# Kernel tuning notes

Hardware: AMD Instinct MI355X
Metric: run time of the kernel (lower is better)

The kernel has to match this reference:

```python
import jax, jax.numpy as jnp
import numpy as np

N_SRC1, N_DST1, N_DST2 = 200000, 50000, 10000
E1, E2 = 2000000, 400000
IN_F, H_F, N_CLS = 128, 256, 47


def setup_inputs() -> dict:
    key = jax.random.key(0)
    ks = jax.random.split(key, 10)
    x = jax.random.normal(ks[0], (N_SRC1, IN_F), dtype=jnp.float32)
    W_self1 = jax.random.normal(ks[1], (IN_F, H_F), dtype=jnp.float32) * (1.0 / np.sqrt(IN_F))
    W_neigh1 = jax.random.normal(ks[2], (IN_F, H_F), dtype=jnp.float32) * (1.0 / np.sqrt(IN_F))
    b1 = jnp.zeros((H_F,), dtype=jnp.float32)
    W_self2 = jax.random.normal(ks[3], (H_F, N_CLS), dtype=jnp.float32) * (1.0 / np.sqrt(H_F))
    W_neigh2 = jax.random.normal(ks[4], (H_F, N_CLS), dtype=jnp.float32) * (1.0 / np.sqrt(H_F))
    b2 = jnp.zeros((N_CLS,), dtype=jnp.float32)
    src1 = jax.random.randint(ks[5], (E1,), 0, N_SRC1, dtype=jnp.int64)
    dst1 = jnp.sort(jax.random.randint(ks[6], (E1,), 0, N_DST1, dtype=jnp.int64))
    src2 = jax.random.randint(ks[7], (E2,), 0, N_DST1, dtype=jnp.int64)
    dst2 = jnp.sort(jax.random.randint(ks[8], (E2,), 0, N_DST2, dtype=jnp.int64))
    return {"x": x, "W_self1": W_self1, "W_neigh1": W_neigh1, "b1": b1,
            "W_self2": W_self2, "W_neigh2": W_neigh2, "b2": b2,
            "src1": src1, "dst1": dst1, "src2": src2, "dst2": dst2,
            "n_dst1": N_DST1, "n_dst2": N_DST2}


def _sage_mean(h_src, h_dst, src, dst, n_dst, W_self, W_neigh, b):
    # mean neighbor aggregation: gather src feats, segment-sum onto dst, divide by in-degree
    msum = jax.ops.segment_sum(h_src[src], dst, num_segments=n_dst)  # [n_dst, F]
    deg = jax.ops.segment_sum(jnp.ones(src.shape, h_src.dtype), dst, num_segments=n_dst)
    h_neigh = msum / jnp.maximum(deg, 1.0)[:, None]
    return h_dst @ W_self + h_neigh @ W_neigh + b


def reference(x, W_self1, W_neigh1, b1, W_self2, W_neigh2, b2,
              src1, dst1, src2, dst2, n_dst1, n_dst2):
    # layer 1 (dst nodes are the prefix of src nodes, DGL MFG convention)
    h = _sage_mean(x, x[:n_dst1], src1, dst1, n_dst1, W_self1, W_neigh1, b1)
    h = jax.nn.relu(h)  # dropout = identity (eval mode)
    # layer 2
    out = _sage_mean(h, h[:n_dst2], src2, dst2, n_dst2, W_self2, W_neigh2, b2)
    return out
```

## Files before the change

kernel.cpp:

```cpp
#include <hip/hip_runtime.h>

constexpr int N_DST1 = 50000;
constexpr int N_DST2 = 10000;
constexpr int E1     = 2000000;
constexpr int E2     = 400000;
constexpr int IN_F   = 128;
constexpr int H_F    = 256;
constexpr int N_CLS  = 47;

constexpr size_t RP1_OFF = 0;
constexpr size_t RP2_OFF = 204800;
constexpr size_t BPS_OFF = 245760;
constexpr size_t BPN_OFF = 311296;
constexpr size_t BP2_OFF = 376832;
constexpr size_t X8_OFF  = 430080;
constexpr size_t HN1_OFF = 26030080;
constexpr size_t HB_OFF  = 38830080;
constexpr size_t H8_OFF  = 64430080;
constexpr size_t HN2_OFF = 77230080;

using f32x4  = __attribute__((ext_vector_type(4))) float;
using f32x2  = __attribute__((ext_vector_type(2))) float;
using short8 = __attribute__((ext_vector_type(8))) short;

__device__ __forceinline__ ushort f2bf(float f) {
    union { float f; unsigned u; } v; v.f = f;
    unsigned u = v.u;
    return (ushort)((u + 0x7fffu + ((u >> 16) & 1u)) >> 16);
}

constexpr int CAST_BLKS = 200000 * IN_F / 8 / 256;
constexpr int PACK_BLKS = 44;
constexpr int RP_BLKS   = (N_DST1 + N_DST2 + 2 + 255) / 256;

__global__ __launch_bounds__(256) void setup_all(
    const float* __restrict__ x, unsigned char* __restrict__ x8,
    const float* __restrict__ Ws1, const float* __restrict__ Wn1,
    const float* __restrict__ Ws2, const float* __restrict__ Wn2,
    ushort* __restrict__ bps, ushort* __restrict__ bpn, ushort* __restrict__ bp2,
    const int* __restrict__ dst1, const int* __restrict__ dst2,
    int* __restrict__ rp1, int* __restrict__ rp2) {
    int b = blockIdx.x;
    if (b < CAST_BLKS) {
        int i = b * 256 + threadIdx.x;
        float4 v0 = ((const float4*)x)[2 * i];
        float4 v1 = ((const float4*)x)[2 * i + 1];
        int p0 = __builtin_amdgcn_cvt_pk_fp8_f32(v0.x, v0.y, 0, false);
        p0     = __builtin_amdgcn_cvt_pk_fp8_f32(v0.z, v0.w, p0, true);
        int p1 = __builtin_amdgcn_cvt_pk_fp8_f32(v1.x, v1.y, 0, false);
        p1     = __builtin_amdgcn_cvt_pk_fp8_f32(v1.z, v1.w, p1, true);
        uint2 o; o.x = (unsigned)p0; o.y = (unsigned)p1;
        ((uint2*)x8)[i] = o;
    } else if (b < CAST_BLKS + PACK_BLKS) {
        int pb = b - CAST_BLKS;
        if (pb < 32) {
            const float* W = (pb < 16) ? Ws1 : Wn1;
            ushort* P      = (pb < 16) ? bps : bpn;
            int idx = (pb & 15) * 256 + threadIdx.x;
            int lane = idx & 63, kb = (idx >> 6) & 3, nb = idx >> 8;
            int n  = nb * 16 + (lane & 15);
            int k0 = kb * 32 + ((lane >> 4) * 8);
            ushort tmp[8];
#pragma unroll
            for (int j = 0; j < 8; ++j) tmp[j] = f2bf(W[(k0 + j) * H_F + n]);
            ((uint4*)P)[idx] = *(uint4*)tmp;
        } else {
            int idx = (pb - 32) * 256 + threadIdx.x;
            if (idx < 3072) {
                int lane = idx & 63, rem = idx >> 6;
                int nb = rem % 3, kb = rem / 3;
                int col = nb * 16 + (lane & 15);
                int k0  = (kb & 7) * 32 + ((lane >> 4) * 8);
                const float* W = (kb < 8) ? Ws2 : Wn2;
                ushort tmp[8];
#pragma unroll
                for (int j = 0; j < 8; ++j)
                    tmp[j] = (col < N_CLS) ? f2bf(W[(k0 + j) * N_CLS + col]) : (ushort)0;
                ((uint4*)bp2)[(kb * 3 + nb) * 64 + lane] = *(uint4*)tmp;
            }
        }
    } else {
        int idx = (b - CAST_BLKS - PACK_BLKS) * 256 + threadIdx.x;
        const int* dst; int* rp; int E; int target;
        if (idx <= N_DST1) { dst = dst1; rp = rp1; E = E1; target = idx; }
        else if (idx <= N_DST1 + 1 + N_DST2) {
            dst = dst2; rp = rp2; E = E2; target = idx - (N_DST1 + 1);
        } else return;
        int lo = 0, hi = E;
        while (lo < hi) {
            int mid = (lo + hi) >> 1;
            if (dst[mid] < target) lo = mid + 1; else hi = mid;
        }
        rp[target] = lo;
    }
}

__global__ __launch_bounds__(64) void agg1b(const unsigned char* __restrict__ x8,
                                            const int* __restrict__ src,
                                            const int* __restrict__ rp,
                                            ushort* __restrict__ hn) {
    int d = blockIdx.x, t = threadIdx.x;
    int s = rp[d], e = rp[d + 1];
    const unsigned* x1 = (const unsigned*)x8;
    int half = t >> 5, li = t & 31;
    float a0 = 0.f, a1 = 0.f, a2 = 0.f, a3 = 0.f;
    int deg = e - s;
    int npairs = deg >> 1;
    int j = 0;
    for (; j + 4 <= npairs; j += 4) {
        int b0 = s + 2 * j;
        int i0 = src[b0],     i1 = src[b0 + 1], i2 = src[b0 + 2], i3 = src[b0 + 3];
        int i4 = src[b0 + 4], i5 = src[b0 + 5], i6 = src[b0 + 6], i7 = src[b0 + 7];
        unsigned v0 = x1[(half ? i1 : i0) * 32 + li];
        unsigned v1 = x1[(half ? i3 : i2) * 32 + li];
        unsigned v2 = x1[(half ? i5 : i4) * 32 + li];
        unsigned v3 = x1[(half ? i7 : i6) * 32 + li];
#pragma unroll
        for (int q = 0; q < 4; ++q) {
            unsigned v = (q == 0) ? v0 : (q == 1) ? v1 : (q == 2) ? v2 : v3;
            f32x2 f0 = __builtin_amdgcn_cvt_pk_f32_fp8((int)v, false);
            f32x2 f1 = __builtin_amdgcn_cvt_pk_f32_fp8((int)v, true);
            a0 += f0[0]; a1 += f0[1]; a2 += f1[0]; a3 += f1[1];
        }
    }
    for (; j < npairs; ++j) {
        int b0 = s + 2 * j;
        int i0 = src[b0], i1 = src[b0 + 1];
        unsigned v = x1[(half ? i1 : i0) * 32 + li];
        f32x2 f0 = __builtin_amdgcn_cvt_pk_f32_fp8((int)v, false);
        f32x2 f1 = __builtin_amdgcn_cvt_pk_f32_fp8((int)v, true);
        a0 += f0[0]; a1 += f0[1]; a2 += f1[0]; a3 += f1[1];
    }
    if (deg & 1) {
        int it = src[e - 1];
        if (half == 0) {
            unsigned v = x1[it * 32 + li];
            f32x2 f0 = __builtin_amdgcn_cvt_pk_f32_fp8((int)v, false);
            f32x2 f1 = __builtin_amdgcn_cvt_pk_f32_fp8((int)v, true);
            a0 += f0[0]; a1 += f0[1]; a2 += f1[0]; a3 += f1[1];
        }
    }
    float c0 = a0 + __shfl(a0, li + 32);
    float c1 = a1 + __shfl(a1, li + 32);
    float c2 = a2 + __shfl(a2, li + 32);
    float c3 = a3 + __shfl(a3, li + 32);
    if (t < 32) {
        float inv = 1.f / fmaxf((float)deg, 1.f);
        uint2 o;
        o.x = (unsigned)f2bf(c0 * inv) | ((unsigned)f2bf(c1 * inv) << 16);
        o.y = (unsigned)f2bf(c2 * inv) | ((unsigned)f2bf(c3 * inv) << 16);
        ((uint2*)hn)[d * 32 + li] = o;
    }
}

__global__ __launch_bounds__(64) void agg2b(const unsigned char* __restrict__ h8,
                                            const int* __restrict__ src,
                                            const int* __restrict__ rp,
                                            ushort* __restrict__ hn) {
    int d = blockIdx.x, t = threadIdx.x;
    int s = rp[d], e = rp[d + 1];
    const uint2* h2 = (const uint2*)h8;
    int half = t >> 5, li = t & 31;
    float a[8] = {};
    int deg = e - s;
    int npairs = deg >> 1;
    int j = 0;
    for (; j + 2 <= npairs; j += 2) {
        int b0 = s + 2 * j;
        int i0 = src[b0], i1 = src[b0 + 1], i2 = src[b0 + 2], i3 = src[b0 + 3];
        uint2 v0 = h2[(half ? i1 : i0) * 32 + li];
        uint2 v1 = h2[(half ? i3 : i2) * 32 + li];
#pragma unroll
        for (int q = 0; q < 2; ++q) {
            uint2 v = q ? v1 : v0;
            f32x2 f0 = __builtin_amdgcn_cvt_pk_f32_fp8((int)v.x, false);
            f32x2 f1 = __builtin_amdgcn_cvt_pk_f32_fp8((int)v.x, true);
            f32x2 f2 = __builtin_amdgcn_cvt_pk_f32_fp8((int)v.y, false);
            f32x2 f3 = __builtin_amdgcn_cvt_pk_f32_fp8((int)v.y, true);
            a[0] += f0[0]; a[1] += f0[1]; a[2] += f1[0]; a[3] += f1[1];
            a[4] += f2[0]; a[5] += f2[1]; a[6] += f3[0]; a[7] += f3[1];
        }
    }
    for (; j < npairs; ++j) {
        int b0 = s + 2 * j;
        int i0 = src[b0], i1 = src[b0 + 1];
        uint2 v = h2[(half ? i1 : i0) * 32 + li];
        f32x2 f0 = __builtin_amdgcn_cvt_pk_f32_fp8((int)v.x, false);
        f32x2 f1 = __builtin_amdgcn_cvt_pk_f32_fp8((int)v.x, true);
        f32x2 f2 = __builtin_amdgcn_cvt_pk_f32_fp8((int)v.y, false);
        f32x2 f3 = __builtin_amdgcn_cvt_pk_f32_fp8((int)v.y, true);
        a[0] += f0[0]; a[1] += f0[1]; a[2] += f1[0]; a[3] += f1[1];
        a[4] += f2[0]; a[5] += f2[1]; a[6] += f3[0]; a[7] += f3[1];
    }
    if (deg & 1) {
        int it = src[e - 1];
        if (half == 0) {
            uint2 v = h2[it * 32 + li];
            f32x2 f0 = __builtin_amdgcn_cvt_pk_f32_fp8((int)v.x, false);
            f32x2 f1 = __builtin_amdgcn_cvt_pk_f32_fp8((int)v.x, true);
            f32x2 f2 = __builtin_amdgcn_cvt_pk_f32_fp8((int)v.y, false);
            f32x2 f3 = __builtin_amdgcn_cvt_pk_f32_fp8((int)v.y, true);
            a[0] += f0[0]; a[1] += f0[1]; a[2] += f1[0]; a[3] += f1[1];
            a[4] += f2[0]; a[5] += f2[1]; a[6] += f3[0]; a[7] += f3[1];
        }
    }
    float c[8];
#pragma unroll
    for (int q = 0; q < 8; ++q) c[q] = a[q] + __shfl(a[q], li + 32);
    if (t < 32) {
        float inv = 1.f / fmaxf((float)deg, 1.f);
        uint4 o;
        o.x = (unsigned)f2bf(c[0] * inv) | ((unsigned)f2bf(c[1] * inv) << 16);
        o.y = (unsigned)f2bf(c[2] * inv) | ((unsigned)f2bf(c[3] * inv) << 16);
        o.z = (unsigned)f2bf(c[4] * inv) | ((unsigned)f2bf(c[5] * inv) << 16);
        o.w = (unsigned)f2bf(c[6] * inv) | ((unsigned)f2bf(c[7] * inv) << 16);
        ((uint4*)hn)[d * 32 + li] = o;
    }
}

__global__ __launch_bounds__(256) void gemm1_mfma(
    const float* __restrict__ x, const ushort* __restrict__ hn1,
    const ushort* __restrict__ BpS, const ushort* __restrict__ BpN,
    const float* __restrict__ b1, ushort* __restrict__ hb,
    unsigned char* __restrict__ h8) {
    __shared__ ushort bsm[16 * 64 * 8];
    int tid = threadIdx.x;
    int wave = tid >> 6, lane = tid & 63;
    int m0 = (blockIdx.x * 4 + wave) * 16;
    int mrow = m0 + (lane & 15);
    bool active = (m0 < N_DST1);
    if (mrow >= N_DST1) mrow = 0;
    int koff = (lane >> 4) * 8;

    f32x4 acc[16];
#pragma unroll
    for (int nb = 0; nb < 16; ++nb) acc[nb] = (f32x4){0.f, 0.f, 0.f, 0.f};

    for (int ph = 0; ph < 2; ++ph) {
        const uint4* Pg = (const uint4*)((ph == 0) ? BpS : BpN);
        const float*  Af = x   + (size_t)mrow * IN_F;
        const ushort* Ah = hn1 + (size_t)mrow * IN_F;
        for (int kb = 0; kb < 4; ++kb) {
            __syncthreads();
#pragma unroll
            for (int i = 0; i < 4; ++i) {
                int u = tid + 256 * i;
                int nb = u >> 6, l6 = u & 63;
                ((uint4*)bsm)[u] = Pg[(nb * 4 + kb) * 64 + l6];
            }
            __syncthreads();
            short8 a;
            if (ph == 0) {
                float4 a0 = *(const float4*)(Af + kb * 32 + koff);
                float4 a1 = *(const float4*)(Af + kb * 32 + koff + 4);
                a[0] = (short)f2bf(a0.x); a[1] = (short)f2bf(a0.y);
                a[2] = (short)f2bf(a0.z); a[3] = (short)f2bf(a0.w);
                a[4] = (short)f2bf(a1.x); a[5] = (short)f2bf(a1.y);
                a[6] = (short)f2bf(a1.z); a[7] = (short)f2bf(a1.w);
            } else {
                a = *(const short8*)(Ah + kb * 32 + koff);
            }
#pragma unroll
            for (int nb = 0; nb < 16; ++nb) {
                short8 b = *(const short8*)&bsm[(nb * 64 + lane) * 8];
                acc[nb] = __builtin_amdgcn_mfma_f32_16x16x32_bf16(a, b, acc[nb], 0, 0, 0);
            }
        }
    }
    if (!active) return;
    int crow0 = m0 + (lane >> 4) * 4;
    int ccol  = lane & 15;
#pragma unroll
    for (int nb = 0; nb < 16; ++nb) {
        float bias = b1[nb * 16 + ccol];
#pragma unroll
        for (int r = 0; r < 4; ++r) {
            int row = crow0 + r;
            if (row < N_DST1) {
                float v = fmaxf(acc[nb][r] + bias, 0.f);
                size_t col = (size_t)nb * 16 + ccol;
                hb[(size_t)row * H_F + col] = f2bf(v);
                int p = __builtin_amdgcn_cvt_pk_fp8_f32(v, v, 0, false);
                h8[(size_t)row * H_F + col] = (unsigned char)(p & 0xff);
            }
        }
    }
}

__global__ __launch_bounds__(256) void gemm2_mfma(
    const ushort* __restrict__ hb, const ushort* __restrict__ hn2,
    const ushort* __restrict__ P2, const float* __restrict__ b2,
    float* __restrict__ out) {
    int tid = threadIdx.x;
    int wave = tid >> 6, lane = tid & 63;
    int m0 = (blockIdx.x * 4 + wave) * 16;
    if (m0 >= N_DST2) return;
    int mrow = m0 + (lane & 15);
    int koff = (lane >> 4) * 8;

    f32x4 acc[3];
#pragma unroll
    for (int nb = 0; nb < 3; ++nb) acc[nb] = (f32x4){0.f, 0.f, 0.f, 0.f};

#pragma unroll
    for (int kb = 0; kb < 16; ++kb) {
        const ushort* A = (kb < 8)
            ? (hb  + (size_t)mrow * H_F + kb * 32 + koff)
            : (hn2 + (size_t)mrow * H_F + (kb - 8) * 32 + koff);
        short8 a = *(const short8*)A;
#pragma unroll
        for (int nb = 0; nb < 3; ++nb) {
            short8 b = *(const short8*)(P2 + ((size_t)(kb * 3 + nb) * 64 + lane) * 8);
            acc[nb] = __builtin_amdgcn_mfma_f32_16x16x32_bf16(a, b, acc[nb], 0, 0, 0);
        }
    }
    int crow0 = m0 + (lane >> 4) * 4;
    int ccol  = lane & 15;
#pragma unroll
    for (int nb = 0; nb < 3; ++nb) {
        int col = nb * 16 + ccol;
        if (col < N_CLS) {
            float bias = b2[col];
#pragma unroll
            for (int r = 0; r < 4; ++r)
                out[(size_t)(crow0 + r) * N_CLS + col] = acc[nb][r] + bias;
        }
    }
}

extern "C" void kernel_launch(void* const* d_in, const int* in_sizes, int n_in,
                              void* d_out, int out_size, void* d_ws, size_t ws_size,
                              hipStream_t stream) {
    const float* x   = (const float*)d_in[0];
    const float* Ws1 = (const float*)d_in[1];
    const float* Wn1 = (const float*)d_in[2];
    const float* b1  = (const float*)d_in[3];
    const float* Ws2 = (const float*)d_in[4];
    const float* Wn2 = (const float*)d_in[5];
    const float* b2  = (const float*)d_in[6];
    const int* src1  = (const int*)d_in[7];
    const int* dst1  = (const int*)d_in[8];
    const int* src2  = (const int*)d_in[9];
    const int* dst2  = (const int*)d_in[10];
    float* out = (float*)d_out;

    char* ws = (char*)d_ws;
    int*           rp1 = (int*)(ws + RP1_OFF);
    int*           rp2 = (int*)(ws + RP2_OFF);
    ushort*        bps = (ushort*)(ws + BPS_OFF);
    ushort*        bpn = (ushort*)(ws + BPN_OFF);
    ushort*        bp2 = (ushort*)(ws + BP2_OFF);
    unsigned char* x8  = (unsigned char*)(ws + X8_OFF);
    ushort*        hn1 = (ushort*)(ws + HN1_OFF);
    ushort*        hb  = (ushort*)(ws + HB_OFF);
    unsigned char* h8  = (unsigned char*)(ws + H8_OFF);
    ushort*        hn2 = (ushort*)(ws + HN2_OFF);

    setup_all<<<CAST_BLKS + PACK_BLKS + RP_BLKS, 256, 0, stream>>>(
        x, x8, Ws1, Wn1, Ws2, Wn2, bps, bpn, bp2, dst1, dst2, rp1, rp2);
    agg1b<<<N_DST1, 64, 0, stream>>>(x8, src1, rp1, hn1);
    gemm1_mfma<<<(N_DST1 / 16 + 3) / 4, 256, 0, stream>>>(x, hn1, bps, bpn, b1, hb, h8);
    agg2b<<<N_DST2, 64, 0, stream>>>(h8, src2, rp2, hn2);
    gemm2_mfma<<<(N_DST2 / 16 + 3) / 4, 256, 0, stream>>>(hb, hn2, bp2, b2, out);
}
```

Measured before the change: 306.6 us.

## Fuse neighbor aggregation into per-layer MFMA GEMM kernels via LDS tiles

Merges the layer-1 aggregation and GEMM into one kernel, and does the same for layer 2. Each wave now aggregates its 16 destination rows one after another into an LDS A-tile, then runs the MFMA GEMM from that tile. This removes the hn1/hn2 global round trips and two kernel launches. The self-feature bf16 copy hb is now written only for the rows layer 2 needs. In exchange, the latency-bound gather runs with far fewer waves in flight (782 blocks of 256 threads instead of 50000 single-wave blocks), and each wave handles its rows serially, so load-latency hiding may suffer.

```diff
diff --git a/kernel.cpp b/kernel.cpp
--- a/kernel.cpp
+++ b/kernel.cpp
@@ -14,10 +14,8 @@
 constexpr size_t BPN_OFF = 311296;
 constexpr size_t BP2_OFF = 376832;
 constexpr size_t X8_OFF  = 430080;
-constexpr size_t HN1_OFF = 26030080;
-constexpr size_t HB_OFF  = 38830080;
-constexpr size_t H8_OFF  = 64430080;
-constexpr size_t HN2_OFF = 77230080;
+constexpr size_t HB_OFF  = 26030080;
+constexpr size_t H8_OFF  = 31150080;
 
 using f32x4  = __attribute__((ext_vector_type(4))) float;
 using f32x2  = __attribute__((ext_vector_type(2))) float;
@@ -95,84 +93,167 @@
     }
 }
 
-__global__ __launch_bounds__(64) void agg1b(const unsigned char* __restrict__ x8,
-                                            const int* __restrict__ src,
-                                            const int* __restrict__ rp,
-                                            ushort* __restrict__ hn) {
-    int d = blockIdx.x, t = threadIdx.x;
-    int s = rp[d], e = rp[d + 1];
+__global__ __launch_bounds__(256) void layer1(
+    const float* __restrict__ x, const unsigned char* __restrict__ x8,
+    const int* __restrict__ src, const int* __restrict__ rp,
+    const ushort* __restrict__ BpS, const ushort* __restrict__ BpN,
+    const float* __restrict__ b1,
+    ushort* __restrict__ hb, unsigned char* __restrict__ h8) {
+    __shared__ ushort At[4][16 * 136];
+    __shared__ ushort bsm[16 * 64 * 8];
+    int tid = threadIdx.x, wave = tid >> 6, lane = tid & 63;
+    int m0 = blockIdx.x * 64 + wave * 16;
+    bool active = (m0 < N_DST1);
+    int half = lane >> 5, li = lane & 31;
+    ushort* Atile = At[wave];
     const unsigned* x1 = (const unsigned*)x8;
-    int half = t >> 5, li = t & 31;
-    float a0 = 0.f, a1 = 0.f, a2 = 0.f, a3 = 0.f;
-    int deg = e - s;
-    int npairs = deg >> 1;
-    int j = 0;
-    for (; j + 4 <= npairs; j += 4) {
-        int b0 = s + 2 * j;
-        int i0 = src[b0],     i1 = src[b0 + 1], i2 = src[b0 + 2], i3 = src[b0 + 3];
-        int i4 = src[b0 + 4], i5 = src[b0 + 5], i6 = src[b0 + 6], i7 = src[b0 + 7];
-        unsigned v0 = x1[(half ? i1 : i0) * 32 + li];
-        unsigned v1 = x1[(half ? i3 : i2) * 32 + li];
-        unsigned v2 = x1[(half ? i5 : i4) * 32 + li];
-        unsigned v3 = x1[(half ? i7 : i6) * 32 + li];
-#pragma unroll
-        for (int q = 0; q < 4; ++q) {
-            unsigned v = (q == 0) ? v0 : (q == 1) ? v1 : (q == 2) ? v2 : v3;
-            f32x2 f0 = __builtin_amdgcn_cvt_pk_f32_fp8((int)v, false);
-            f32x2 f1 = __builtin_amdgcn_cvt_pk_f32_fp8((int)v, true);
-            a0 += f0[0]; a1 += f0[1]; a2 += f1[0]; a3 += f1[1];
-        }
-    }
-    for (; j < npairs; ++j) {
-        int b0 = s + 2 * j;
-        int i0 = src[b0], i1 = src[b0 + 1];
-        unsigned v = x1[(half ? i1 : i0) * 32 + li];
-        f32x2 f0 = __builtin_amdgcn_cvt_pk_f32_fp8((int)v, false);
-        f32x2 f1 = __builtin_amdgcn_cvt_pk_f32_fp8((int)v, true);
-        a0 += f0[0]; a1 += f0[1]; a2 += f1[0]; a3 += f1[1];
-    }
-    if (deg & 1) {
-        int it = src[e - 1];
-        if (half == 0) {
-            unsigned v = x1[it * 32 + li];
-            f32x2 f0 = __builtin_amdgcn_cvt_pk_f32_fp8((int)v, false);
-            f32x2 f1 = __builtin_amdgcn_cvt_pk_f32_fp8((int)v, true);
-            a0 += f0[0]; a1 += f0[1]; a2 += f1[0]; a3 += f1[1];
-        }
-    }
-    float c0 = a0 + __shfl(a0, li + 32);
-    float c1 = a1 + __shfl(a1, li + 32);
-    float c2 = a2 + __shfl(a2, li + 32);
-    float c3 = a3 + __shfl(a3, li + 32);
-    if (t < 32) {
-        float inv = 1.f / fmaxf((float)deg, 1.f);
-        uint2 o;
-        o.x = (unsigned)f2bf(c0 * inv) | ((unsigned)f2bf(c1 * inv) << 16);
-        o.y = (unsigned)f2bf(c2 * inv) | ((unsigned)f2bf(c3 * inv) << 16);
-        ((uint2*)hn)[d * 32 + li] = o;
-    }
-}
-
-__global__ __launch_bounds__(64) void agg2b(const unsigned char* __restrict__ h8,
-                                            const int* __restrict__ src,
-                                            const int* __restrict__ rp,
-                                            ushort* __restrict__ hn) {
-    int d = blockIdx.x, t = threadIdx.x;
-    int s = rp[d], e = rp[d + 1];
+
+    if (active) {
+        for (int m = 0; m < 16; ++m) {
+            int d = m0 + m;
+            int s = rp[d], e = rp[d + 1];
+            int deg = e - s;
+            float a0 = 0.f, a1 = 0.f, a2 = 0.f, a3 = 0.f;
+            int npairs = deg >> 1;
+            int j = 0;
+            for (; j + 4 <= npairs; j += 4) {
+                int b0 = s + 2 * j;
+                int i0 = src[b0],     i1 = src[b0 + 1], i2 = src[b0 + 2], i3 = src[b0 + 3];
+                int i4 = src[b0 + 4], i5 = src[b0 + 5], i6 = src[b0 + 6], i7 = src[b0 + 7];
+                unsigned v0 = x1[(half ? i1 : i0) * 32 + li];
+                unsigned v1 = x1[(half ? i3 : i2) * 32 + li];
+                unsigned v2 = x1[(half ? i5 : i4) * 32 + li];
+                unsigned v3 = x1[(half ? i7 : i6) * 32 + li];
+#pragma unroll
+                for (int q = 0; q < 4; ++q) {
+                    unsigned v = (q == 0) ? v0 : (q == 1) ? v1 : (q == 2) ? v2 : v3;
+                    f32x2 f0 = __builtin_amdgcn_cvt_pk_f32_fp8((int)v, false);
+                    f32x2 f1 = __builtin_amdgcn_cvt_pk_f32_fp8((int)v, true);
+                    a0 += f0[0]; a1 += f0[1]; a2 += f1[0]; a3 += f1[1];
+                }
+            }
+            for (; j < npairs; ++j) {
+                int b0 = s + 2 * j;
+                int i0 = src[b0], i1 = src[b0 + 1];
+                unsigned v = x1[(half ? i1 : i0) * 32 + li];
+                f32x2 f0 = __builtin_amdgcn_cvt_pk_f32_fp8((int)v, false);
+                f32x2 f1 = __builtin_amdgcn_cvt_pk_f32_fp8((int)v, true);
+                a0 += f0[0]; a1 += f0[1]; a2 += f1[0]; a3 += f1[1];
+            }
+            if ((deg & 1) && half == 0) {
+                unsigned v = x1[src[e - 1] * 32 + li];
+                f32x2 f0 = __builtin_amdgcn_cvt_pk_f32_fp8((int)v, false);
+                f32x2 f1 = __builtin_amdgcn_cvt_pk_f32_fp8((int)v, true);
+                a0 += f0[0]; a1 += f0[1]; a2 += f1[0]; a3 += f1[1];
+            }
+            float c0 = a0 + __shfl(a0, li + 32);
+            float c1 = a1 + __shfl(a1, li + 32);
+            float c2 = a2 + __shfl(a2, li + 32);
+            float c3 = a3 + __shfl(a3, li + 32);
+            if (lane < 32) {
+                float inv = 1.f / fmaxf((float)deg, 1.f);
+                uint2 o;
+                o.x = (unsigned)f2bf(c0 * inv) | ((unsigned)f2bf(c1 * inv) << 16);
+                o.y = (unsigned)f2bf(c2 * inv) | ((unsigned)f2bf(c3 * inv) << 16);
+                *(uint2*)&Atile[m * 136 + li * 4] = o;
+            }
+        }
+    }
+
+    f32x4 acc[16];
+#pragma unroll
+    for (int nb = 0; nb < 16; ++nb) acc[nb] = (f32x4){0.f, 0.f, 0.f, 0.f};
+    int mloc = lane & 15;
+    int koff = (lane >> 4) * 8;
+    const float* Af = x + (size_t)(m0 + mloc) * IN_F;
+
+    for (int ph = 0; ph < 2; ++ph) {
+        const uint4* Pg = (const uint4*)((ph == 0) ? BpS : BpN);
+        for (int kb = 0; kb < 4; ++kb) {
+            __syncthreads();
+#pragma unroll
+            for (int i = 0; i < 4; ++i) {
+                int u = tid + 256 * i;
+                int nb = u >> 6, l6 = u & 63;
+                ((uint4*)bsm)[u] = Pg[(nb * 4 + kb) * 64 + l6];
+            }
+            __syncthreads();
+            short8 a;
+            if (ph == 0) {
+                float4 q0 = *(const float4*)(Af + kb * 32 + koff);
+                float4 q1 = *(const float4*)(Af + kb * 32 + koff + 4);
+                a[0] = (short)f2bf(q0.x); a[1] = (short)f2bf(q0.y);
+                a[2] = (short)f2bf(q0.z); a[3] = (short)f2bf(q0.w);
+                a[4] = (short)f2bf(q1.x); a[5] = (short)f2bf(q1.y);
+                a[6] = (short)f2bf(q1.z); a[7] = (short)f2bf(q1.w);
+            } else {
+                a = *(const short8*)&Atile[mloc * 136 + kb * 32 + koff];
+            }
+#pragma unroll
+            for (int nb = 0; nb < 16; ++nb) {
+                short8 b = *(const short8*)&bsm[(nb * 64 + lane) * 8];
+                acc[nb] = __builtin_amdgcn_mfma_f32_16x16x32_bf16(a, b, acc[nb], 0, 0, 0);
+            }
+        }
+    }
+    if (!active) return;
+    int crow0 = m0 + (lane >> 4) * 4;
+    int ccol  = lane & 15;
+#pragma unroll
+    for (int nb = 0; nb < 16; ++nb) {
+        float bias = b1[nb * 16 + ccol];
+#pragma unroll
+        for (int r = 0; r < 4; ++r) {
+            float v = fmaxf(acc[nb][r] + bias, 0.f);
+            int row = crow0 + r;
+            size_t col = (size_t)nb * 16 + ccol;
+            int p = __builtin_amdgcn_cvt_pk_fp8_f32(v, v, 0, false);
+            h8[(size_t)row * H_F + col] = (unsigned char)(p & 0xff);
+            if (row < N_DST2) hb[(size_t)row * H_F + col] = f2bf(v);
+        }
+    }
+}
+
+__global__ __launch_bounds__(256) void layer2(
+    const ushort* __restrict__ hb, const unsigned char* __restrict__ h8,
+    const int* __restrict__ src, const int* __restrict__ rp,
+    const ushort* __restrict__ P2, const float* __restrict__ b2,
+    float* __restrict__ out) {
+    __shared__ ushort At[4][16 * 264];
+    int tid = threadIdx.x, wave = tid >> 6, lane = tid & 63;
+    int m0 = blockIdx.x * 64 + wave * 16;
+    if (m0 >= N_DST2) return;
+    int half = lane >> 5, li = lane & 31;
+    ushort* Atile = At[wave];
     const uint2* h2 = (const uint2*)h8;
-    int half = t >> 5, li = t & 31;
-    float a[8] = {};
-    int deg = e - s;
-    int npairs = deg >> 1;
-    int j = 0;
-    for (; j + 2 <= npairs; j += 2) {
-        int b0 = s + 2 * j;
-        int i0 = src[b0], i1 = src[b0 + 1], i2 = src[b0 + 2], i3 = src[b0 + 3];
-        uint2 v0 = h2[(half ? i1 : i0) * 32 + li];
-        uint2 v1 = h2[(half ? i3 : i2) * 32 + li];
-#pragma unroll
-        for (int q = 0; q < 2; ++q) {
-            uint2 v = q ? v1 : v0;
+
+    for (int m = 0; m < 16; ++m) {
+        int d = m0 + m;
+        int s = rp[d], e = rp[d + 1];
+        int deg = e - s;
+        float a[8] = {};
+        int npairs = deg >> 1;
+        int j = 0;
+        for (; j + 2 <= npairs; j += 2) {
+            int b0 = s + 2 * j;
+            int i0 = src[b0], i1 = src[b0 + 1], i2 = src[b0 + 2], i3 = src[b0 + 3];
+            uint2 v0 = h2[(half ? i1 : i0) * 32 + li];
+            uint2 v1 = h2[(half ? i3 : i2) * 32 + li];
+#pragma unroll
+            for (int q = 0; q < 2; ++q) {
+                uint2 v = q ? v1 : v0;
+                f32x2 f0 = __builtin_amdgcn_cvt_pk_f32_fp8((int)v.x, false);
+                f32x2 f1 = __builtin_amdgcn_cvt_pk_f32_fp8((int)v.x, true);
+                f32x2 f2 = __builtin_amdgcn_cvt_pk_f32_fp8((int)v.y, false);
+                f32x2 f3 = __builtin_amdgcn_cvt_pk_f32_fp8((int)v.y, true);
+                a[0] += f0[0]; a[1] += f0[1]; a[2] += f1[0]; a[3] += f1[1];
+                a[4] += f2[0]; a[5] += f2[1]; a[6] += f3[0]; a[7] += f3[1];
+            }
+        }
+        for (; j < npairs; ++j) {
+            int b0 = s + 2 * j;
+            int i0 = src[b0], i1 = src[b0 + 1];
+            uint2 v = h2[(half ? i1 : i0) * 32 + li];
             f32x2 f0 = __builtin_amdgcn_cvt_pk_f32_fp8((int)v.x, false);
             f32x2 f1 = __builtin_amdgcn_cvt_pk_f32_fp8((int)v.x, true);
             f32x2 f2 = __builtin_amdgcn_cvt_pk_f32_fp8((int)v.y, false);
@@ -180,22 +261,8 @@
             a[0] += f0[0]; a[1] += f0[1]; a[2] += f1[0]; a[3] += f1[1];
             a[4] += f2[0]; a[5] += f2[1]; a[6] += f3[0]; a[7] += f3[1];
         }
-    }
-    for (; j < npairs; ++j) {
-        int b0 = s + 2 * j;
-        int i0 = src[b0], i1 = src[b0 + 1];
-        uint2 v = h2[(half ? i1 : i0) * 32 + li];
-        f32x2 f0 = __builtin_amdgcn_cvt_pk_f32_fp8((int)v.x, false);
-        f32x2 f1 = __builtin_amdgcn_cvt_pk_f32_fp8((int)v.x, true);
-        f32x2 f2 = __builtin_amdgcn_cvt_pk_f32_fp8((int)v.y, false);
-        f32x2 f3 = __builtin_amdgcn_cvt_pk_f32_fp8((int)v.y, true);
-        a[0] += f0[0]; a[1] += f0[1]; a[2] += f1[0]; a[3] += f1[1];
-        a[4] += f2[0]; a[5] += f2[1]; a[6] += f3[0]; a[7] += f3[1];
-    }
-    if (deg & 1) {
-        int it = src[e - 1];
-        if (half == 0) {
-            uint2 v = h2[it * 32 + li];
+        if ((deg & 1) && half == 0) {
+            uint2 v = h2[src[e - 1] * 32 + li];
             f32x2 f0 = __builtin_amdgcn_cvt_pk_f32_fp8((int)v.x, false);
             f32x2 f1 = __builtin_amdgcn_cvt_pk_f32_fp8((int)v.x, true);
             f32x2 f2 = __builtin_amdgcn_cvt_pk_f32_fp8((int)v.y, false);
@@ -203,111 +270,31 @@
             a[0] += f0[0]; a[1] += f0[1]; a[2] += f1[0]; a[3] += f1[1];
             a[4] += f2[0]; a[5] += f2[1]; a[6] += f3[0]; a[7] += f3[1];
         }
-    }
-    float c[8];
-#pragma unroll
-    for (int q = 0; q < 8; ++q) c[q] = a[q] + __shfl(a[q], li + 32);
-    if (t < 32) {
-        float inv = 1.f / fmaxf((float)deg, 1.f);
-        uint4 o;
-        o.x = (unsigned)f2bf(c[0] * inv) | ((unsigned)f2bf(c[1] * inv) << 16);
-        o.y = (unsigned)f2bf(c[2] * inv) | ((unsigned)f2bf(c[3] * inv) << 16);
-        o.z = (unsigned)f2bf(c[4] * inv) | ((unsigned)f2bf(c[5] * inv) << 16);
-        o.w = (unsigned)f2bf(c[6] * inv) | ((unsigned)f2bf(c[7] * inv) << 16);
-        ((uint4*)hn)[d * 32 + li] = o;
-    }
-}
-
-__global__ __launch_bounds__(256) void gemm1_mfma(
-    const float* __restrict__ x, const ushort* __restrict__ hn1,
-    const ushort* __restrict__ BpS, const ushort* __restrict__ BpN,
-    const float* __restrict__ b1, ushort* __restrict__ hb,
-    unsigned char* __restrict__ h8) {
-    __shared__ ushort bsm[16 * 64 * 8];
-    int tid = threadIdx.x;
-    int wave = tid >> 6, lane = tid & 63;
-    int m0 = (blockIdx.x * 4 + wave) * 16;
-    int mrow = m0 + (lane & 15);
-    bool active = (m0 < N_DST1);
-    if (mrow >= N_DST1) mrow = 0;
+        float c[8];
+#pragma unroll
+        for (int q = 0; q < 8; ++q) c[q] = a[q] + __shfl(a[q], li + 32);
+        if (lane < 32) {
+            float inv = 1.f / fmaxf((float)deg, 1.f);
+            uint4 o;
+            o.x = (unsigned)f2bf(c[0] * inv) | ((unsigned)f2bf(c[1] * inv) << 16);
+            o.y = (unsigned)f2bf(c[2] * inv) | ((unsigned)f2bf(c[3] * inv) << 16);
+            o.z = (unsigned)f2bf(c[4] * inv) | ((unsigned)f2bf(c[5] * inv) << 16);
+            o.w = (unsigned)f2bf(c[6] * inv) | ((unsigned)f2bf(c[7] * inv) << 16);
+            *(uint4*)&Atile[m * 264 + li * 8] = o;
+        }
+    }
+
+    f32x4 acc[3];
+#pragma unroll
+    for (int nb = 0; nb < 3; ++nb) acc[nb] = (f32x4){0.f, 0.f, 0.f, 0.f};
+    int mloc = lane & 15;
     int koff = (lane >> 4) * 8;
-
-    f32x4 acc[16];
-#pragma unroll
-    for (int nb = 0; nb < 16; ++nb) acc[nb] = (f32x4){0.f, 0.f, 0.f, 0.f};
-
-    for (int ph = 0; ph < 2; ++ph) {
-        const uint4* Pg = (const uint4*)((ph == 0) ? BpS : BpN);
-        const float*  Af = x   + (size_t)mrow * IN_F;
-        const ushort* Ah = hn1 + (size_t)mrow * IN_F;
-        for (int kb = 0; kb < 4; ++kb) {
-            __syncthreads();
-#pragma unroll
-            for (int i = 0; i < 4; ++i) {
-                int u = tid + 256 * i;
-                int nb = u >> 6, l6 = u & 63;
-                ((uint4*)bsm)[u] = Pg[(nb * 4 + kb) * 64 + l6];
-            }
-            __syncthreads();
-            short8 a;
-            if (ph == 0) {
-                float4 a0 = *(const float4*)(Af + kb * 32 + koff);
-                float4 a1 = *(const float4*)(Af + kb * 32 + koff + 4);
-                a[0] = (short)f2bf(a0.x); a[1] = (short)f2bf(a0.y);
-                a[2] = (short)f2bf(a0.z); a[3] = (short)f2bf(a0.w);
-                a[4] = (short)f2bf(a1.x); a[5] = (short)f2bf(a1.y);
-                a[6] = (short)f2bf(a1.z); a[7] = (short)f2bf(a1.w);
-            } else {
-                a = *(const short8*)(Ah + kb * 32 + koff);
-            }
-#pragma unroll
-            for (int nb = 0; nb < 16; ++nb) {
-                short8 b = *(const short8*)&bsm[(nb * 64 + lane) * 8];
-                acc[nb] = __builtin_amdgcn_mfma_f32_16x16x32_bf16(a, b, acc[nb], 0, 0, 0);
-            }
-        }
-    }
-    if (!active) return;
-    int crow0 = m0 + (lane >> 4) * 4;
-    int ccol  = lane & 15;
-#pragma unroll
-    for (int nb = 0; nb < 16; ++nb) {
-        float bias = b1[nb * 16 + ccol];
-#pragma unroll
-        for (int r = 0; r < 4; ++r) {
-            int row = crow0 + r;
-            if (row < N_DST1) {
-                float v = fmaxf(acc[nb][r] + bias, 0.f);
-                size_t col = (size_t)nb * 16 + ccol;
-                hb[(size_t)row * H_F + col] = f2bf(v);
-                int p = __builtin_amdgcn_cvt_pk_fp8_f32(v, v, 0, false);
-                h8[(size_t)row * H_F + col] = (unsigned char)(p & 0xff);
-            }
-        }
-    }
-}
-
-__global__ __launch_bounds__(256) void gemm2_mfma(
-    const ushort* __restrict__ hb, const ushort* __restrict__ hn2,
-    const ushort* __restrict__ P2, const float* __restrict__ b2,
-    float* __restrict__ out) {
-    int tid = threadIdx.x;
-    int wave = tid >> 6, lane = tid & 63;
-    int m0 = (blockIdx.x * 4 + wave) * 16;
-    if (m0 >= N_DST2) return;
-    int mrow = m0 + (lane & 15);
-    int koff = (lane >> 4) * 8;
-
-    f32x4 acc[3];
-#pragma unroll
-    for (int nb = 0; nb < 3; ++nb) acc[nb] = (f32x4){0.f, 0.f, 0.f, 0.f};
-
+    const ushort* Ah = hb + (size_t)(m0 + mloc) * H_F;
 #pragma unroll
     for (int kb = 0; kb < 16; ++kb) {
-        const ushort* A = (kb < 8)
-            ? (hb  + (size_t)mrow * H_F + kb * 32 + koff)
-            : (hn2 + (size_t)mrow * H_F + (kb - 8) * 32 + koff);
-        short8 a = *(const short8*)A;
+        short8 a;
+        if (kb < 8) a = *(const short8*)(Ah + kb * 32 + koff);
+        else        a = *(const short8*)&Atile[mloc * 264 + (kb - 8) * 32 + koff];
 #pragma unroll
         for (int nb = 0; nb < 3; ++nb) {
             short8 b = *(const short8*)(P2 + ((size_t)(kb * 3 + nb) * 64 + lane) * 8);
@@ -351,15 +338,13 @@
     ushort*        bpn = (ushort*)(ws + BPN_OFF);
     ushort*        bp2 = (ushort*)(ws + BP2_OFF);
     unsigned char* x8  = (unsigned char*)(ws + X8_OFF);
-    ushort*        hn1 = (ushort*)(ws + HN1_OFF);
     ushort*        hb  = (ushort*)(ws + HB_OFF);
     unsigned char* h8  = (unsigned char*)(ws + H8_OFF);
-    ushort*        hn2 = (ushort*)(ws + HN2_OFF);
 
     setup_all<<<CAST_BLKS + PACK_BLKS + RP_BLKS, 256, 0, stream>>>(
         x, x8, Ws1, Wn1, Ws2, Wn2, bps, bpn, bp2, dst1, dst2, rp1, rp2);
-    agg1b<<<N_DST1, 64, 0, stream>>>(x8, src1, rp1, hn1);
-    gemm1_mfma<<<(N_DST1 / 16 + 3) / 4, 256, 0, stream>>>(x, hn1, bps, bpn, b1, hb, h8);
-    agg2b<<<N_DST2, 64, 0, stream>>>(h8, src2, rp2, hn2);
-    gemm2_mfma<<<(N_DST2 / 16 + 3) / 4, 256, 0, stream>>>(hb, hn2, bp2, b2, out);
-}
+    layer1<<<(N_DST1 + 63) / 64, 256, 0, stream>>>(
+        x, x8, src1, rp1, bps, bpn, b1, hb, h8);
+    layer2<<<(N_DST2 + 63) / 64, 256, 0, stream>>>(
+        hb, h8, src2, rp2, bp2, b2, out);
+}
```

Measured after the change: 492.5 us. 60.6% more time.
